# Kernel optimization log

Hardware: AMD Instinct MI355X
Metric: run time of the kernel (lower is better)

The kernel has to match this reference:

```python
import jax, jax.numpy as jnp
import numpy as np

M_DIM = 1024
H_DIM = 1024
NEG = -1e9


def setup_inputs() -> dict:
    key = jax.random.key(0)
    ks = jax.random.split(key, 9)
    B, S = 4, 2048
    q = jax.random.normal(ks[0], (B, S, M_DIM), dtype=jnp.float32)
    k = jax.random.normal(ks[1], (B, S, M_DIM), dtype=jnp.float32)
    v = jax.random.normal(ks[2], (B, S, M_DIM), dtype=jnp.float32)
    attention_mask = jnp.ones((B, S), dtype=jnp.int32)
    sc = 1.0 / np.sqrt(M_DIM)
    Wq_w = jax.random.normal(ks[3], (H_DIM, M_DIM), dtype=jnp.float32) * sc
    Wq_b = jnp.zeros((H_DIM,), dtype=jnp.float32)
    Wk_w = jax.random.normal(ks[4], (H_DIM, M_DIM), dtype=jnp.float32) * sc
    Wk_b = jnp.zeros((H_DIM,), dtype=jnp.float32)
    Wv_w = jax.random.normal(ks[5], (H_DIM, M_DIM), dtype=jnp.float32) * sc
    Wv_b = jnp.zeros((H_DIM,), dtype=jnp.float32)
    return {"q": q, "k": k, "v": v, "attention_mask": attention_mask,
            "Wq_w": Wq_w, "Wq_b": Wq_b, "Wk_w": Wk_w, "Wk_b": Wk_b,
            "Wv_w": Wv_w, "Wv_b": Wv_b}


def reference(q, k, v, attention_mask, Wq_w, Wq_b, Wk_w, Wk_b, Wv_w, Wv_b):
    # Linear projections (torch Linear: x @ W.T + b)
    qh = jnp.einsum('bsm,hm->bsh', q, Wq_w) + Wq_b
    kh = jnp.einsum('bsm,hm->bsh', k, Wk_w) + Wk_b
    vh = jnp.einsum('bsm,hm->bsh', v, Wv_w) + Wv_b
    # Scaled dot-product scores: [B, Sq, Sk]
    scores = jnp.einsum('bqh,bkh->bqk', qh, kh) / jnp.sqrt(jnp.float32(H_DIM))
    # Padding mask: attention_mask [B, Sk] -> [B, 1, Sk]
    pad = attention_mask.astype(bool)[:, None, :]
    scores = jnp.where(pad, scores, NEG)
    # Causal mask (apply_mask=True)
    Sq, Sk = scores.shape[1], scores.shape[2]
    causal = jnp.tril(jnp.ones((Sq, Sk), dtype=bool))
    scores = jnp.where(causal[None, :, :], scores, NEG)
    attn = jax.nn.softmax(scores, axis=-1)
    out = jnp.einsum('bqk,bkh->bqh', attn, vh)
    # dropout is identity in eval mode
    return out
```

## Files before the change

kernel.cpp:

```cpp
#include <hip/hip_runtime.h>
#include <stdint.h>


typedef __attribute__((ext_vector_type(8))) short s8v;
typedef __attribute__((ext_vector_type(4))) float f4v;

__device__ __forceinline__ unsigned short f2bf(float f) {
    union { float f; unsigned u; } v; v.f = f;
    unsigned u = v.u;
    u = u + 0x7fffu + ((u >> 16) & 1u);
    return (unsigned short)(u >> 16);
}

__device__ __forceinline__ void gld_lds16(const void* gptr, void* lptr) {
    __builtin_amdgcn_global_load_lds(
        (const __attribute__((address_space(1))) unsigned int*)(uintptr_t)gptr,
        (__attribute__((address_space(3))) unsigned int*)(unsigned int)(uintptr_t)lptr,
        16, 0, 0);
}

__global__ __launch_bounds__(256) void convert_all(
    const float* __restrict__ q, const float* __restrict__ k, const float* __restrict__ v,
    const float* __restrict__ wq, const float* __restrict__ wk, const float* __restrict__ wv,
    unsigned short* __restrict__ qb, unsigned short* __restrict__ kb, unsigned short* __restrict__ vb,
    unsigned short* __restrict__ wqb, unsigned short* __restrict__ wkb, unsigned short* __restrict__ wvb,
    float* __restrict__ l)
{
    int b = blockIdx.x;
    if (b >= 27648) {
        int li = (b - 27648) * 256 + threadIdx.x;
        l[li] = 0.f;
        return;
    }
    const float* src; unsigned short* dst; int blk;
    if (b < 8192)       { src = q;  dst = qb;  blk = b; }
    else if (b < 16384) { src = k;  dst = kb;  blk = b - 8192; }
    else if (b < 24576) { src = v;  dst = vb;  blk = b - 16384; }
    else if (b < 25600) { src = wq; dst = wqb; blk = b - 24576; }
    else if (b < 26624) { src = wk; dst = wkb; blk = b - 25600; }
    else                { src = wv; dst = wvb; blk = b - 26624; }
    size_t idx = (size_t)blk * 1024 + (size_t)threadIdx.x * 4;
    float4 f = *(const float4*)(src + idx);
    ushort4 o = make_ushort4(f2bf(f.x), f2bf(f.y), f2bf(f.z), f2bf(f.w));
    *(ushort4*)(dst + idx) = o;
}

__device__ __forceinline__ void gemm_tiles(
    const unsigned short* __restrict__ A, int lda,
    const unsigned short* __restrict__ Bt, int ldb,
    int m0, int n0, int kTiles,
    unsigned short* As, unsigned short* Bs,
    f4v acc[4][4])
{
    const int t    = threadIdx.x;
    const int lane = t & 63;
    const int wave = t >> 6;
    const int wm   = (wave >> 1) * 64;
    const int wn   = (wave & 1) * 64;
    const int l15  = lane & 15;
    const int quad = lane >> 4;

    const int c0 = t, c1 = t + 256;
    unsigned short* As0 = As + (c0 & ~63) * 8;
    unsigned short* As1 = As + (c1 & ~63) * 8;
    unsigned short* Bs0 = Bs + (c0 & ~63) * 8;
    unsigned short* Bs1 = Bs + (c1 & ~63) * 8;
    const unsigned short* Ag0 = A  + (size_t)(m0 + (c0 >> 2)) * lda + (c0 & 3) * 8;
    const unsigned short* Ag1 = A  + (size_t)(m0 + (c1 >> 2)) * lda + (c1 & 3) * 8;
    const unsigned short* Bg0 = Bt + (size_t)(n0 + (c0 >> 2)) * ldb + (c0 & 3) * 8;
    const unsigned short* Bg1 = Bt + (size_t)(n0 + (c1 >> 2)) * ldb + (c1 & 3) * 8;

    const unsigned short* a_base = As + quad * 8;
    const unsigned short* b_base = Bs + quad * 8;

    gld_lds16(Ag0, As0);
    gld_lds16(Ag1, As1);
    gld_lds16(Bg0, Bs0);
    gld_lds16(Bg1, Bs1);

    for (int kt = 0; kt < kTiles; ++kt) {
        __syncthreads();
        Ag0 += 32; Ag1 += 32; Bg0 += 32; Bg1 += 32;
        if (kt + 1 < kTiles) {
            const int nb = ((kt + 1) & 1) * 4096;
            gld_lds16(Ag0, As0 + nb);
            gld_lds16(Ag1, As1 + nb);
            gld_lds16(Bg0, Bs0 + nb);
            gld_lds16(Bg1, Bs1 + nb);
        }
        const int cb = (kt & 1) * 4096;
        s8v af[4], bf[4];
        #pragma unroll
        for (int i = 0; i < 4; ++i)
            af[i] = *(const s8v*)(a_base + cb + (wm + i * 16 + l15) * 32);
        #pragma unroll
        for (int j = 0; j < 4; ++j)
            bf[j] = *(const s8v*)(b_base + cb + (wn + j * 16 + l15) * 32);
        #pragma unroll
        for (int i = 0; i < 4; ++i)
            #pragma unroll
            for (int j = 0; j < 4; ++j)
                acc[i][j] = __builtin_amdgcn_mfma_f32_16x16x32_bf16(af[i], bf[j], acc[i][j], 0, 0, 0);
    }
}

#define ACC_INIT  f4v acc[4][4]; { f4v z = {0.f,0.f,0.f,0.f}; \
    _Pragma("unroll") for (int i = 0; i < 4; ++i) \
    _Pragma("unroll") for (int j = 0; j < 4; ++j) acc[i][j] = z; }

#define LANE_VARS \
    const int lane = threadIdx.x & 63; const int wave = threadIdx.x >> 6; \
    const int wm = (wave >> 1) * 64;  const int wn = (wave & 1) * 64; \
    const int l15 = lane & 15;        const int quad = lane >> 4;

__global__ __launch_bounds__(256) void proj_kernel(
    const unsigned short* __restrict__ qb, const unsigned short* __restrict__ wqb,
    const float* __restrict__ bq, unsigned short* __restrict__ QH,
    const unsigned short* __restrict__ kb, const unsigned short* __restrict__ wkb,
    const float* __restrict__ bk, unsigned short* __restrict__ KH,
    const unsigned short* __restrict__ vb, const unsigned short* __restrict__ wvb,
    const float* __restrict__ bv, unsigned short* __restrict__ VHT)
{
    const int z = blockIdx.z;
    const unsigned short* X; const unsigned short* W; const float* bias; unsigned short* Y;
    if (z == 0)      { X = qb; W = wqb; bias = bq; Y = QH; }
    else if (z == 1) { X = kb; W = wkb; bias = bk; Y = KH; }
    else             { X = vb; W = wvb; bias = bv; Y = VHT; }

    __shared__ __align__(16) unsigned short As[2 * 128 * 32];
    __shared__ __align__(16) unsigned short Bs[2 * 128 * 32];
    const int m0 = blockIdx.x * 128;
    const int n0 = blockIdx.y * 128;
    ACC_INIT;
    gemm_tiles(X, 1024, W, 1024, m0, n0, 32, As, Bs, acc);
    LANE_VARS;
    #pragma unroll
    for (int i = 0; i < 4; ++i) {
        int row = m0 + wm + i * 16 + quad * 4;
        #pragma unroll
        for (int j = 0; j < 4; ++j) {
            int col = n0 + wn + j * 16 + l15;
            float bvv = bias[col];
            if (z != 2) {
                #pragma unroll
                for (int r = 0; r < 4; ++r)
                    Y[(size_t)(row + r) * 1024 + col] = f2bf(acc[i][j][r] + bvv);
            } else {
                int bb = row >> 11;
                int s  = row & 2047;
                ushort4 o = make_ushort4(f2bf(acc[i][j][0] + bvv), f2bf(acc[i][j][1] + bvv),
                                         f2bf(acc[i][j][2] + bvv), f2bf(acc[i][j][3] + bvv));
                *(ushort4*)(Y + (size_t)bb * (1024 * 2048) + (size_t)col * 2048 + s) = o;
            }
        }
    }
}

__global__ __launch_bounds__(256) void score_kernel(
    const unsigned short* __restrict__ QH, const unsigned short* __restrict__ KH,
    const int* __restrict__ mask, unsigned short* __restrict__ P, float* __restrict__ lsum)
{
    const int b = blockIdx.y;
    int tq = blockIdx.x;
    int qt = 0;
    while ((qt + 1) * (qt + 2) / 2 <= tq) ++qt;
    const int kt = tq - qt * (qt + 1) / 2;

    __shared__ __align__(16) unsigned short As[2 * 128 * 32];
    __shared__ __align__(16) unsigned short Bs[2 * 128 * 32];
    const unsigned short* A  = QH + (size_t)b * 2048 * 1024;
    const unsigned short* Bt = KH + (size_t)b * 2048 * 1024;
    unsigned short* Pb = P + (size_t)b * 2048 * 2048;
    float* lb = lsum + b * 2048;
    const int* mb = mask + b * 2048;
    const int m0 = qt * 128, n0 = kt * 128;
    ACC_INIT;
    gemm_tiles(A, 1024, Bt, 1024, m0, n0, 32, As, Bs, acc);
    LANE_VARS;
    float rs[4][4];
    #pragma unroll
    for (int i = 0; i < 4; ++i)
        #pragma unroll
        for (int r = 0; r < 4; ++r) rs[i][r] = 0.f;
    #pragma unroll
    for (int i = 0; i < 4; ++i) {
        int qbase = m0 + wm + i * 16 + quad * 4;
        #pragma unroll
        for (int j = 0; j < 4; ++j) {
            int kg = n0 + wn + j * 16 + l15;
            int mv = mb[kg];
            #pragma unroll
            for (int r = 0; r < 4; ++r) {
                float s = acc[i][j][r] * 0.03125f;
                float p = (mv && (kg <= qbase + r)) ? __expf(s) : 0.f;
                Pb[(size_t)(qbase + r) * 2048 + kg] = f2bf(p);
                rs[i][r] += p;
            }
        }
    }
    #pragma unroll
    for (int i = 0; i < 4; ++i)
        #pragma unroll
        for (int r = 0; r < 4; ++r) {
            float v_ = rs[i][r];
            v_ += __shfl_xor(v_, 1);
            v_ += __shfl_xor(v_, 2);
            v_ += __shfl_xor(v_, 4);
            v_ += __shfl_xor(v_, 8);
            if (l15 == 0)
                atomicAdd(&lb[m0 + wm + i * 16 + quad * 4 + r], v_);
        }
}

__constant__ int pv_qt[24] = {15,15, 7,14,14,13,13, 6,12,12,11,11, 5,10,10, 9, 9, 4, 8, 8, 3, 2, 1, 0};
__constant__ int pv_ks[24] = { 0,32, 0, 0,30, 0,28, 0, 0,26, 0,24, 0, 0,22, 0,20, 0, 0,18, 0, 0, 0, 0};
__constant__ int pv_kc[24] = {32,32,32,30,30,28,28,28,26,26,24,24,24,22,22,20,20,20,18,18,16,12, 8, 4};

__global__ __launch_bounds__(256) void pv_kernel(
    const unsigned short* __restrict__ P, const unsigned short* __restrict__ VHT,
    const float* __restrict__ lsum, float* __restrict__ Out, float* __restrict__ Part)
{
    const int nt = blockIdx.x, y = blockIdx.y, b = blockIdx.z;
    const int qt = pv_qt[y], kstart = pv_ks[y], kcount = pv_kc[y];

    __shared__ __align__(16) unsigned short As[2 * 128 * 32];
    __shared__ __align__(16) unsigned short Bs[2 * 128 * 32];
    const unsigned short* A  = P   + (size_t)b * 2048 * 2048 + (size_t)kstart * 32;
    const unsigned short* Bt = VHT + (size_t)b * 1024 * 2048 + (size_t)kstart * 32;
    const float* lb = lsum + b * 2048;
    const int m0 = qt * 128, n0 = nt * 128;
    ACC_INIT;
    gemm_tiles(A, 2048, Bt, 2048, m0, n0, kcount, As, Bs, acc);
    LANE_VARS;
    float* dst; int rowoff;
    if (kstart == 0) { dst = Out  + (size_t)b * 2048 * 1024; rowoff = 0; }
    else             { dst = Part + (size_t)b * 1024 * 1024; rowoff = -1024; }
    #pragma unroll
    for (int i = 0; i < 4; ++i) {
        int q0 = m0 + wm + i * 16 + quad * 4;
        float inv[4];
        #pragma unroll
        for (int r = 0; r < 4; ++r) inv[r] = 1.0f / lb[q0 + r];
        #pragma unroll
        for (int j = 0; j < 4; ++j) {
            int h = n0 + wn + j * 16 + l15;
            #pragma unroll
            for (int r = 0; r < 4; ++r)
                dst[(size_t)(q0 + r + rowoff) * 1024 + h] = acc[i][j][r] * inv[r];
        }
    }
}

__global__ __launch_bounds__(256) void add_partial(
    float4* __restrict__ Out4, const float4* __restrict__ Part4)
{
    int i = blockIdx.x * 256 + threadIdx.x;
    int b = i >> 18;
    int rem = i & 262143;
    int oi = b * 524288 + 262144 + rem;
    float4 o = Out4[oi], p = Part4[i];
    o.x += p.x; o.y += p.y; o.z += p.z; o.w += p.w;
    Out4[oi] = o;
}

extern "C" void kernel_launch(void* const* d_in, const int* in_sizes, int n_in,
                              void* d_out, int out_size, void* d_ws, size_t ws_size,
                              hipStream_t stream)
{
    const float* q    = (const float*)d_in[0];
    const float* k    = (const float*)d_in[1];
    const float* v    = (const float*)d_in[2];
    const int*   mask = (const int*)d_in[3];
    const float* Wq   = (const float*)d_in[4];
    const float* bq   = (const float*)d_in[5];
    const float* Wk   = (const float*)d_in[6];
    const float* bk   = (const float*)d_in[7];
    const float* Wv   = (const float*)d_in[8];
    const float* bv   = (const float*)d_in[9];
    float* out = (float*)d_out;

    char* ws = (char*)d_ws;
    size_t off = 0;
    auto take = [&](size_t bytes) { char* p = ws + off; off += (bytes + 255) & ~(size_t)255; return p; };
    unsigned short* qb  = (unsigned short*)take(8192ull * 1024 * 2);
    unsigned short* kb  = (unsigned short*)take(8192ull * 1024 * 2);
    unsigned short* vb  = (unsigned short*)take(8192ull * 1024 * 2);
    unsigned short* wqb = (unsigned short*)take(1024ull * 1024 * 2);
    unsigned short* wkb = (unsigned short*)take(1024ull * 1024 * 2);
    unsigned short* wvb = (unsigned short*)take(1024ull * 1024 * 2);
    unsigned short* QH  = (unsigned short*)take(8192ull * 1024 * 2);
    unsigned short* KH  = (unsigned short*)take(8192ull * 1024 * 2);
    unsigned short* VHT = (unsigned short*)take(8192ull * 1024 * 2);
    unsigned short* P   = (unsigned short*)take(4ull * 2048 * 2048 * 2);
    float*          l   = (float*)take(4ull * 2048 * 4);
    float*          Part = (float*)qb;

    convert_all<<<27680, 256, 0, stream>>>(q, k, v, Wq, Wk, Wv,
                                           qb, kb, vb, wqb, wkb, wvb, l);
    proj_kernel<<<dim3(64, 8, 3), 256, 0, stream>>>(qb, wqb, bq, QH,
                                                    kb, wkb, bk, KH,
                                                    vb, wvb, bv, VHT);
    score_kernel<<<dim3(136, 4), 256, 0, stream>>>(QH, KH, mask, P, l);
    pv_kernel<<<dim3(8, 24, 4), 256, 0, stream>>>(P, VHT, l, out, Part);
    add_partial<<<4096, 256, 0, stream>>>((float4*)out, (const float4*)Part);
}
```

Before: 312.1 us.

## Rewrite projection GEMM as 256x256 tile, 8-wave, pipelined with swizzled LDS

The projection kernel moves from 128x128 tiles with 4 waves to 256x256 tiles with 8 waves and a K-step of 64. LDS is double buffered and the layout is XOR-swizzled. Global-to-LDS loads for the next stage are split into halves and interleaved between four MFMA phases, using explicit barriers, waitcnt and setprio. The goal is more data reuse per tile and better overlap of memory traffic with MFMA work, at the cost of more registers, more LDS (128KB) and fewer blocks (384 across three projections).

```diff
diff --git a/kernel.cpp b/kernel.cpp
--- a/kernel.cpp
+++ b/kernel.cpp
@@ -113,7 +113,7 @@
     const int wm = (wave >> 1) * 64;  const int wn = (wave & 1) * 64; \
     const int l15 = lane & 15;        const int quad = lane >> 4;
 
-__global__ __launch_bounds__(256) void proj_kernel(
+__global__ __launch_bounds__(512, 2) void proj_kernel(
     const unsigned short* __restrict__ qb, const unsigned short* __restrict__ wqb,
     const float* __restrict__ bq, unsigned short* __restrict__ QH,
     const unsigned short* __restrict__ kb, const unsigned short* __restrict__ wkb,
@@ -127,29 +127,154 @@
     else if (z == 1) { X = kb; W = wkb; bias = bk; Y = KH; }
     else             { X = vb; W = wvb; bias = bv; Y = VHT; }
 
-    __shared__ __align__(16) unsigned short As[2 * 128 * 32];
-    __shared__ __align__(16) unsigned short Bs[2 * 128 * 32];
-    const int m0 = blockIdx.x * 128;
-    const int n0 = blockIdx.y * 128;
-    ACC_INIT;
-    gemm_tiles(X, 1024, W, 1024, m0, n0, 32, As, Bs, acc);
-    LANE_VARS;
+    __shared__ __align__(16) unsigned short As[2 * 256 * 64];
+    __shared__ __align__(16) unsigned short Bs[2 * 256 * 64];
+
+    const int t    = threadIdx.x;
+    const int lane = t & 63;
+    const int w    = t >> 6;
+    const int wm   = (w >> 2) * 128;
+    const int wn   = (w & 3) * 64;
+    const int l15  = lane & 15;
+    const int quad = lane >> 4;
+    const int m0   = blockIdx.x * 256;
+    const int n0   = blockIdx.y * 256;
+    enum { KT = 16 };
+
+    const int r0 = t >> 3;
+    const int sw = (t & 7) ^ (r0 & 7);
+    const unsigned short* gA = X + (size_t)(m0 + r0) * 1024 + sw * 8;
+    const unsigned short* gB = W + (size_t)(n0 + r0) * 1024 + sw * 8;
+    unsigned short* lA = As + (t & ~63) * 8;
+    unsigned short* lB = Bs + (t & ~63) * 8;
+
+#define PSTAGE_A(b, h, kt) { \
+    gld_lds16(gA + (size_t)(h) * 131072 + (kt) * 64,         lA + (b) * 16384 + (h) * 8192); \
+    gld_lds16(gA + (size_t)(h) * 131072 + 65536 + (kt) * 64, lA + (b) * 16384 + (h) * 8192 + 4096); }
+#define PSTAGE_B(b, h, kt) { \
+    gld_lds16(gB + (size_t)(h) * 131072 + (kt) * 64,         lB + (b) * 16384 + (h) * 8192); \
+    gld_lds16(gB + (size_t)(h) * 131072 + 65536 + (kt) * 64, lB + (b) * 16384 + (h) * 8192 + 4096); }
+
+    const int aoff = (wm + l15) * 64;
+    const int boff = (wn + l15) * 64;
+    const int seg0 = ((quad    ) ^ (l15 & 7)) * 8;
+    const int seg1 = ((quad | 4) ^ (l15 & 7)) * 8;
+
+    f4v acc[8][4];
+    { f4v zz = {0.f, 0.f, 0.f, 0.f};
+      #pragma unroll
+      for (int i = 0; i < 8; ++i)
+        #pragma unroll
+        for (int j = 0; j < 4; ++j) acc[i][j] = zz; }
+    s8v a[8], b0[4], b1[4];
+
+    PSTAGE_A(0, 0, 0); PSTAGE_A(0, 1, 0); PSTAGE_B(0, 0, 0); PSTAGE_B(0, 1, 0);
+    PSTAGE_B(1, 0, 1); PSTAGE_A(1, 0, 1);
+    asm volatile("s_waitcnt vmcnt(4)" ::: "memory");
+    __builtin_amdgcn_s_barrier();
+
+    for (int kt = 0; kt < KT; ++kt) {
+        const int p  = kt & 1;
+        const int np = p ^ 1;
+        const unsigned short* Ar = As + p * 16384 + aoff;
+        const unsigned short* Br = Bs + p * 16384 + boff;
+
+        #pragma unroll
+        for (int i = 0; i < 4; ++i) {
+            a[i * 2]     = *(const s8v*)(Ar + i * 1024 + seg0);
+            a[i * 2 + 1] = *(const s8v*)(Ar + i * 1024 + seg1);
+        }
+        #pragma unroll
+        for (int j = 0; j < 2; ++j) {
+            b0[j * 2]     = *(const s8v*)(Br + j * 1024 + seg0);
+            b0[j * 2 + 1] = *(const s8v*)(Br + j * 1024 + seg1);
+        }
+        if (kt + 1 < KT) PSTAGE_A(np, 1, kt + 1);
+        __builtin_amdgcn_s_barrier();
+        asm volatile("s_waitcnt lgkmcnt(0)" ::: "memory");
+        __builtin_amdgcn_s_setprio(1);
+        #pragma unroll
+        for (int i = 0; i < 4; ++i)
+            #pragma unroll
+            for (int j = 0; j < 2; ++j) {
+                acc[i][j] = __builtin_amdgcn_mfma_f32_16x16x32_bf16(a[i*2],   b0[j*2],   acc[i][j], 0, 0, 0);
+                acc[i][j] = __builtin_amdgcn_mfma_f32_16x16x32_bf16(a[i*2+1], b0[j*2+1], acc[i][j], 0, 0, 0);
+            }
+        __builtin_amdgcn_s_setprio(0);
+        __builtin_amdgcn_s_barrier();
+
+        #pragma unroll
+        for (int j = 0; j < 2; ++j) {
+            b1[j * 2]     = *(const s8v*)(Br + 2048 + j * 1024 + seg0);
+            b1[j * 2 + 1] = *(const s8v*)(Br + 2048 + j * 1024 + seg1);
+        }
+        if (kt + 1 < KT) PSTAGE_B(np, 1, kt + 1);
+        __builtin_amdgcn_s_barrier();
+        asm volatile("s_waitcnt lgkmcnt(0)" ::: "memory");
+        __builtin_amdgcn_s_setprio(1);
+        #pragma unroll
+        for (int i = 0; i < 4; ++i)
+            #pragma unroll
+            for (int j = 0; j < 2; ++j) {
+                acc[i][2+j] = __builtin_amdgcn_mfma_f32_16x16x32_bf16(a[i*2],   b1[j*2],   acc[i][2+j], 0, 0, 0);
+                acc[i][2+j] = __builtin_amdgcn_mfma_f32_16x16x32_bf16(a[i*2+1], b1[j*2+1], acc[i][2+j], 0, 0, 0);
+            }
+        __builtin_amdgcn_s_setprio(0);
+        __builtin_amdgcn_s_barrier();
+
+        #pragma unroll
+        for (int i = 0; i < 4; ++i) {
+            a[i * 2]     = *(const s8v*)(Ar + 4096 + i * 1024 + seg0);
+            a[i * 2 + 1] = *(const s8v*)(Ar + 4096 + i * 1024 + seg1);
+        }
+        if (kt + 2 < KT) PSTAGE_B(p, 0, kt + 2);
+        __builtin_amdgcn_s_barrier();
+        asm volatile("s_waitcnt lgkmcnt(0)" ::: "memory");
+        __builtin_amdgcn_s_setprio(1);
+        #pragma unroll
+        for (int i = 0; i < 4; ++i)
+            #pragma unroll
+            for (int j = 0; j < 2; ++j) {
+                acc[4+i][2+j] = __builtin_amdgcn_mfma_f32_16x16x32_bf16(a[i*2],   b1[j*2],   acc[4+i][2+j], 0, 0, 0);
+                acc[4+i][2+j] = __builtin_amdgcn_mfma_f32_16x16x32_bf16(a[i*2+1], b1[j*2+1], acc[4+i][2+j], 0, 0, 0);
+            }
+        __builtin_amdgcn_s_setprio(0);
+        __builtin_amdgcn_s_barrier();
+
+        if (kt + 2 < KT) PSTAGE_A(p, 0, kt + 2);
+        __builtin_amdgcn_s_barrier();
+        __builtin_amdgcn_s_setprio(1);
+        #pragma unroll
+        for (int i = 0; i < 4; ++i)
+            #pragma unroll
+            for (int j = 0; j < 2; ++j) {
+                acc[4+i][j] = __builtin_amdgcn_mfma_f32_16x16x32_bf16(a[i*2],   b0[j*2],   acc[4+i][j], 0, 0, 0);
+                acc[4+i][j] = __builtin_amdgcn_mfma_f32_16x16x32_bf16(a[i*2+1], b0[j*2+1], acc[4+i][j], 0, 0, 0);
+            }
+        __builtin_amdgcn_s_setprio(0);
+        if (kt + 2 < KT) { asm volatile("s_waitcnt vmcnt(4)" ::: "memory"); }
+        else             { asm volatile("s_waitcnt vmcnt(0)" ::: "memory"); }
+        __builtin_amdgcn_s_barrier();
+    }
+#undef PSTAGE_A
+#undef PSTAGE_B
+
     #pragma unroll
-    for (int i = 0; i < 4; ++i) {
-        int row = m0 + wm + i * 16 + quad * 4;
-        #pragma unroll
-        for (int j = 0; j < 4; ++j) {
-            int col = n0 + wn + j * 16 + l15;
+    for (int ig = 0; ig < 8; ++ig) {
+        int row = m0 + wm + ig * 16 + quad * 4;
+        #pragma unroll
+        for (int jg = 0; jg < 4; ++jg) {
+            int col = n0 + wn + jg * 16 + l15;
             float bvv = bias[col];
             if (z != 2) {
                 #pragma unroll
                 for (int r = 0; r < 4; ++r)
-                    Y[(size_t)(row + r) * 1024 + col] = f2bf(acc[i][j][r] + bvv);
+                    Y[(size_t)(row + r) * 1024 + col] = f2bf(acc[ig][jg][r] + bvv);
             } else {
                 int bb = row >> 11;
                 int s  = row & 2047;
-                ushort4 o = make_ushort4(f2bf(acc[i][j][0] + bvv), f2bf(acc[i][j][1] + bvv),
-                                         f2bf(acc[i][j][2] + bvv), f2bf(acc[i][j][3] + bvv));
+                ushort4 o = make_ushort4(f2bf(acc[ig][jg][0] + bvv), f2bf(acc[ig][jg][1] + bvv),
+                                         f2bf(acc[ig][jg][2] + bvv), f2bf(acc[ig][jg][3] + bvv));
                 *(ushort4*)(Y + (size_t)bb * (1024 * 2048) + (size_t)col * 2048 + s) = o;
             }
         }
@@ -297,7 +422,7 @@
 
     convert_all<<<27680, 256, 0, stream>>>(q, k, v, Wq, Wk, Wv,
                                            qb, kb, vb, wqb, wkb, wvb, l);
-    proj_kernel<<<dim3(64, 8, 3), 256, 0, stream>>>(qb, wqb, bq, QH,
+    proj_kernel<<<dim3(32, 4, 3), 512, 0, stream>>>(qb, wqb, bq, QH,
                                                     kb, wkb, bk, KH,
                                                     vb, wvb, bv, VHT);
     score_kernel<<<dim3(136, 4), 256, 0, stream>>>(QH, KH, mask, P, l);
```

After: 311.1 us. Within noise of the previous version (-0.3%).
